# Optimization experiments

Measured on AMD Instinct MI355X. Metric: run time of the kernel, lower is better.

Reference implementation:

```python
import jax, jax.numpy as jnp
import numpy as np

NEG_SLOPE = 0.2


def _attn_layer(x, src, dst, W, a, n_nodes):
    # x: (N, Cin), W: (Cout, Cin) torch Linear convention, a: (2*Cout,)
    h = x @ W.T                                  # (N, Cout)
    H = h.shape[-1]
    # cat([x_i, x_j]) @ a  ==  h[dst] @ a[:H] + h[src] @ a[H:]
    s_i = h @ a[:H]                              # (N,)
    s_j = h @ a[H:]                              # (N,)
    score = s_i[dst] + s_j[src]                  # (E,)
    alpha = jax.nn.leaky_relu(score, NEG_SLOPE)
    # segment softmax over destination nodes
    amax = jax.ops.segment_max(alpha, dst, num_segments=n_nodes)
    amax = jnp.where(jnp.isfinite(amax), amax, 0.0)
    ex = jnp.exp(alpha - amax[dst])
    denom = jax.ops.segment_sum(ex, dst, num_segments=n_nodes)
    alpha = ex / denom[dst]                      # (E,)
    msg = h[src] * alpha[:, None]                # (E, Cout)
    sums = jax.ops.segment_sum(msg, dst, num_segments=n_nodes)
    cnt = jax.ops.segment_sum(jnp.ones_like(alpha), dst, num_segments=n_nodes)
    return sums / jnp.maximum(cnt, 1.0)[:, None]  # mean aggregation


def setup_inputs() -> dict:
    key = jax.random.key(0)
    ks = jax.random.split(key, 8)
    B, N, C, H, E = 16, 2048, 256, 256, 262144
    NT = B * N
    temporal_features = jax.random.normal(ks[0], (B, N, C), dtype=jnp.float32)
    edge_index = jax.random.randint(ks[1], (2, E), 0, NT, dtype=jnp.int64)
    sc = 1.0 / np.sqrt(C)
    W1 = jax.random.normal(ks[2], (H, C), dtype=jnp.float32) * sc
    a1 = jax.random.normal(ks[3], (2 * H,), dtype=jnp.float32) * sc
    W2 = jax.random.normal(ks[4], (H, H), dtype=jnp.float32) * sc
    a2 = jax.random.normal(ks[5], (2 * H,), dtype=jnp.float32) * sc
    W3 = jax.random.normal(ks[6], (H, H), dtype=jnp.float32) * sc
    a3 = jax.random.normal(ks[7], (2 * H,), dtype=jnp.float32) * sc
    return {"temporal_features": temporal_features, "edge_index": edge_index,
            "W1": W1, "a1": a1, "W2": W2, "a2": a2, "W3": W3, "a3": a3}


def reference(temporal_features, edge_index, W1, a1, W2, a2, W3, a3):
    B, N, C = temporal_features.shape
    n_nodes = B * N
    src, dst = edge_index[0], edge_index[1]  # x_j = x[src], x_i = x[dst]
    x = temporal_features.reshape(n_nodes, C)
    for W, a in ((W1, a1), (W2, a2), (W3, a3)):
        x = _attn_layer(x, src, dst, W, a, n_nodes)
        x = jax.nn.elu(x)
    return x.reshape(B, N, -1)
```

## Files before the change

### kernel.cpp

```cpp
#include <hip/hip_runtime.h>
#include <math.h>
#include <stdint.h>


typedef float f32x4 __attribute__((ext_vector_type(4)));
typedef _Float16 f16x8 __attribute__((ext_vector_type(8)));
typedef _Float16 f16x4 __attribute__((ext_vector_type(4)));

#define LDSPAD 40


__global__ __launch_bounds__(256) void convert_f16(const float* __restrict__ src,
                                                   _Float16* __restrict__ dstp)
{
    const int i = (blockIdx.x * 256 + threadIdx.x) * 8;
    float4 a = *(const float4*)&src[i];
    float4 b = *(const float4*)&src[i + 4];
    f16x8 o = {(_Float16)a.x, (_Float16)a.y, (_Float16)a.z, (_Float16)a.w,
               (_Float16)b.x, (_Float16)b.y, (_Float16)b.z, (_Float16)b.w};
    *(f16x8*)&dstp[i] = o;
}


__global__ __launch_bounds__(256) void gemm_f16(const _Float16* __restrict__ X,
                                                const _Float16* __restrict__ Wh,
                                                const float* __restrict__ avec,
                                                _Float16* __restrict__ Hout,
                                                float* __restrict__ si,
                                                float* __restrict__ sj)
{
    __shared__ __align__(16) unsigned char smem[64 * LDSPAD * 2 + 256 * LDSPAD * 2];
    _Float16* Xs = (_Float16*)smem;
    _Float16* Wl = (_Float16*)(smem + 64 * LDSPAD * 2);
    float*    Es = (float*)smem;

    const int tid  = threadIdx.x;
    const int lane = tid & 63;
    const int w    = tid >> 6;
    const int ln   = lane & 15;
    const int kq   = lane >> 4;
    const int m0   = blockIdx.x * 64;

    f32x4 acc[4][4] = {};

    const int sr = tid >> 2;
    const int sc = tid & 3;
    const _Float16* Xrow = X  + (size_t)(m0 + sr) * 256;
    const _Float16* Wrow = Wh + (size_t)tid * 256;

    for (int k0 = 0; k0 < 256; k0 += 32) {
        f16x8 xv = *(const f16x8*)&Xrow[k0 + sc * 8];
        *(f16x8*)&Xs[sr * LDSPAD + sc * 8] = xv;
        f16x8 w0 = *(const f16x8*)&Wrow[k0 + 0];
        f16x8 w1 = *(const f16x8*)&Wrow[k0 + 8];
        f16x8 w2 = *(const f16x8*)&Wrow[k0 + 16];
        f16x8 w3 = *(const f16x8*)&Wrow[k0 + 24];
        *(f16x8*)&Wl[tid * LDSPAD + 0]  = w0;
        *(f16x8*)&Wl[tid * LDSPAD + 8]  = w1;
        *(f16x8*)&Wl[tid * LDSPAD + 16] = w2;
        *(f16x8*)&Wl[tid * LDSPAD + 24] = w3;
        __syncthreads();

        f16x8 af[4], bf[4];
#pragma unroll
        for (int i = 0; i < 4; ++i)
            af[i] = *(const f16x8*)&Xs[(i * 16 + ln) * LDSPAD + kq * 8];
#pragma unroll
        for (int j = 0; j < 4; ++j)
            bf[j] = *(const f16x8*)&Wl[(w * 64 + j * 16 + ln) * LDSPAD + kq * 8];
#pragma unroll
        for (int i = 0; i < 4; ++i)
#pragma unroll
            for (int j = 0; j < 4; ++j)
                acc[i][j] = __builtin_amdgcn_mfma_f32_16x16x32_f16(af[i], bf[j], acc[i][j], 0, 0, 0);
        __syncthreads();
    }

    const int er = tid >> 4;
    const int ec = tid & 15;
    for (int i = 0; i < 4; ++i) {
#pragma unroll
        for (int j = 0; j < 4; ++j) {
            const int col = w * 64 + j * 16 + ln;
#pragma unroll
            for (int q = 0; q < 4; ++q)
                Es[(kq * 4 + q) * 260 + col] = acc[i][j][q];
        }
        __syncthreads();
        const int grow = m0 + i * 16 + er;
        float d0 = 0.f, d1 = 0.f;
#pragma unroll
        for (int c4 = 0; c4 < 4; ++c4) {
            const int col = ec * 4 + c4 * 64;
            f32x4 v  = *(const f32x4*)&Es[er * 260 + col];
            f16x4 hv = {(_Float16)v[0], (_Float16)v[1], (_Float16)v[2], (_Float16)v[3]};
            *(f16x4*)&Hout[(size_t)grow * 256 + col] = hv;
            f32x4 al = *(const f32x4*)&avec[col];
            f32x4 ah = *(const f32x4*)&avec[256 + col];
            d0 += v[0] * al[0] + v[1] * al[1] + v[2] * al[2] + v[3] * al[3];
            d1 += v[0] * ah[0] + v[1] * ah[1] + v[2] * ah[2] + v[3] * ah[3];
        }
#pragma unroll
        for (int d = 8; d; d >>= 1) {
            d0 += __shfl_xor(d0, d);
            d1 += __shfl_xor(d1, d);
        }
        if (ec == 0) { si[grow] = d0; sj[grow] = d1; }
        __syncthreads();
    }
}


__global__ void zero_int(int* p, int n)
{
    int i = blockIdx.x * blockDim.x + threadIdx.x;
    if (i < n) p[i] = 0;
}

__global__ void hist_kernel(const int* __restrict__ dst, int* __restrict__ cnt, int E)
{
    int e = blockIdx.x * blockDim.x + threadIdx.x;
    if (e < E) atomicAdd(&cnt[dst[e]], 1);
}

__global__ __launch_bounds__(1024) void scan_part(const int* __restrict__ cnt,
                                                  int* __restrict__ off,
                                                  int* __restrict__ bsum)
{
    __shared__ int buf[1024];
    const int tid = threadIdx.x;
    const int g = blockIdx.x * 1024 + tid;
    int v = cnt[g];
    buf[tid] = v;
    __syncthreads();
#pragma unroll
    for (int d = 1; d < 1024; d <<= 1) {
        int t = (tid >= d) ? buf[tid - d] : 0;
        __syncthreads();
        buf[tid] += t;
        __syncthreads();
    }
    off[g] = buf[tid] - v;
    if (tid == 1023) bsum[blockIdx.x] = buf[1023];
}

__global__ void scan_bsum(int* bsum, int nb)
{
    __shared__ int b[64];
    const int tid = threadIdx.x;
    b[tid] = (tid < nb) ? bsum[tid] : 0;
    __syncthreads();
    if (tid == 0) {
        int a = 0;
        for (int i = 0; i < nb; ++i) { int t = b[i]; b[i] = a; a += t; }
    }
    __syncthreads();
    if (tid < nb) bsum[tid] = b[tid];
}

__global__ __launch_bounds__(1024) void scan_add(const int* __restrict__ bsum,
                                                 int* __restrict__ off,
                                                 int* __restrict__ cursor,
                                                 int NT, int E)
{
    const int tid = threadIdx.x;
    const int g = blockIdx.x * 1024 + tid;
    int v = off[g] + bsum[blockIdx.x];
    off[g] = v;
    cursor[g] = v;
    if (g == 0) off[NT] = E;
}

__global__ void scatter_kernel(const int* __restrict__ src,
                               const int* __restrict__ dst,
                               int* __restrict__ cursor,
                               int* __restrict__ ssrc, int E)
{
    int e = blockIdx.x * blockDim.x + threadIdx.x;
    if (e < E) {
        int p = atomicAdd(&cursor[dst[e]], 1);
        ssrc[p] = src[e];
    }
}


__device__ __forceinline__ float bcast_f(float x, int l)
{
    return __uint_as_float(__builtin_amdgcn_readlane(__float_as_uint(x), l));
}

template <int F16OUT>
__global__ __launch_bounds__(256) void aggregate(const _Float16* __restrict__ Hh,
                                                 const float* __restrict__ si,
                                                 const float* __restrict__ sj,
                                                 const int* __restrict__ off,
                                                 const int* __restrict__ ssrc,
                                                 void* __restrict__ outv,
                                                 int n_nodes)
{
    const int v = (blockIdx.x * 256 + threadIdx.x) >> 6;
    const int lane = threadIdx.x & 63;
    if (v >= n_nodes) return;

    const int e0 = off[v], e1 = off[v + 1];
    const int deg = e1 - e0;
    f32x4 acc = {0.f, 0.f, 0.f, 0.f};

    if (deg > 0 && deg <= 64) {
        const float siv = si[v];
        const int idx = e0 + lane;
        const bool on = idx < e1;
        int s = 0;
        float scv = -1e30f;
        if (on) {
            s = ssrc[idx];
            float t = siv + sj[s];
            scv = (t >= 0.f) ? t : 0.2f * t;
        }
        float m = scv;
#pragma unroll
        for (int d = 32; d; d >>= 1) m = fmaxf(m, __shfl_xor(m, d));
        float wv = on ? __expf(scv - m) : 0.f;
        float den = wv;
#pragma unroll
        for (int d = 32; d; d >>= 1) den += __shfl_xor(den, d);

        const int c4 = lane * 4;
        for (int eo = 0; eo < deg; eo += 4) {
            const int l1 = (eo + 1 < 63) ? eo + 1 : 63;
            const int l2 = (eo + 2 < 63) ? eo + 2 : 63;
            const int l3 = (eo + 3 < 63) ? eo + 3 : 63;
            const int s0 = __builtin_amdgcn_readlane(s, eo);
            const int s1 = __builtin_amdgcn_readlane(s, l1);
            const int s2 = __builtin_amdgcn_readlane(s, l2);
            const int s3 = __builtin_amdgcn_readlane(s, l3);
            const float w0 = bcast_f(wv, eo);
            const float w1 = bcast_f(wv, l1);
            const float w2 = bcast_f(wv, l2);
            const float w3 = bcast_f(wv, l3);
            const f16x4 v0 = *(const f16x4*)&Hh[(size_t)s0 * 256 + c4];
            const f16x4 v1 = *(const f16x4*)&Hh[(size_t)s1 * 256 + c4];
            const f16x4 v2 = *(const f16x4*)&Hh[(size_t)s2 * 256 + c4];
            const f16x4 v3 = *(const f16x4*)&Hh[(size_t)s3 * 256 + c4];
#pragma unroll
            for (int q = 0; q < 4; ++q)
                acc[q] += w0 * (float)v0[q] + w1 * (float)v1[q]
                        + w2 * (float)v2[q] + w3 * (float)v3[q];
        }
        const float inv = 1.f / (den * (float)deg);
#pragma unroll
        for (int q = 0; q < 4; ++q) acc[q] *= inv;
    } else if (deg > 64) {
        const float siv = si[v];
        float m = -1e30f;
        for (int b = e0 + lane; b < e1; b += 64) {
            float t = siv + sj[ssrc[b]];
            t = (t >= 0.f) ? t : 0.2f * t;
            m = fmaxf(m, t);
        }
#pragma unroll
        for (int d = 32; d; d >>= 1) m = fmaxf(m, __shfl_xor(m, d));
        float den = 0.f;
        for (int b = e0 + lane; b < e1; b += 64) {
            float t = siv + sj[ssrc[b]];
            t = (t >= 0.f) ? t : 0.2f * t;
            den += __expf(t - m);
        }
#pragma unroll
        for (int d = 32; d; d >>= 1) den += __shfl_xor(den, d);
        for (int e = e0; e < e1; ++e) {
            const int s = ssrc[e];
            float t = siv + sj[s];
            t = (t >= 0.f) ? t : 0.2f * t;
            const float wgt = __expf(t - m);
            const f16x4 hv = *(const f16x4*)&Hh[(size_t)s * 256 + lane * 4];
#pragma unroll
            for (int q = 0; q < 4; ++q) acc[q] += wgt * (float)hv[q];
        }
        const float inv = 1.f / (den * (float)deg);
#pragma unroll
        for (int q = 0; q < 4; ++q) acc[q] *= inv;
    }

    float4 o;
    o.x = (acc[0] > 0.f) ? acc[0] : (__expf(acc[0]) - 1.f);
    o.y = (acc[1] > 0.f) ? acc[1] : (__expf(acc[1]) - 1.f);
    o.z = (acc[2] > 0.f) ? acc[2] : (__expf(acc[2]) - 1.f);
    o.w = (acc[3] > 0.f) ? acc[3] : (__expf(acc[3]) - 1.f);
    if (F16OUT) {
        f16x4 oh = {(_Float16)o.x, (_Float16)o.y, (_Float16)o.z, (_Float16)o.w};
        *(f16x4*)&((_Float16*)outv)[(size_t)v * 256 + lane * 4] = oh;
    } else {
        *(float4*)&((float*)outv)[(size_t)v * 256 + lane * 4] = o;
    }
}


extern "C" void kernel_launch(void* const* d_in, const int* in_sizes, int n_in,
                              void* d_out, int out_size, void* d_ws, size_t ws_size,
                              hipStream_t stream)
{
    const float* x0 = (const float*)d_in[0];
    const int*   ei = (const int*)d_in[1];
    const float* Ws[3] = {(const float*)d_in[2], (const float*)d_in[4], (const float*)d_in[6]};
    const float* as[3] = {(const float*)d_in[3], (const float*)d_in[5], (const float*)d_in[7]};
    float* out = (float*)d_out;

    const int NT = in_sizes[0] / 256;
    const int E  = in_sizes[1] / 2;
    const int* srcI = ei;
    const int* dstI = ei + E;

    _Float16* Hh = (_Float16*)d_ws;
    _Float16* Xh = Hh + (size_t)NT * 256;
    float* si    = (float*)(Xh + (size_t)NT * 256);
    float* sj    = si + NT;
    int* cnt     = (int*)(sj + NT);
    int* off     = cnt + NT;
    int* cursor  = off + NT + 1;
    int* ssrc    = cursor + NT;
    int* bsum    = ssrc + E;
    _Float16* Wh = (_Float16*)(((uintptr_t)(bsum + 64) + 255) & ~(uintptr_t)255);

    for (int l = 0; l < 3; ++l)
        convert_f16<<<32, 256, 0, stream>>>(Ws[l], Wh + (size_t)l * 65536);
    convert_f16<<<NT * 256 / 2048, 256, 0, stream>>>(x0, Xh);

    zero_int<<<(NT + 255) / 256, 256, 0, stream>>>(cnt, NT);
    hist_kernel<<<(E + 255) / 256, 256, 0, stream>>>(dstI, cnt, E);
    scan_part<<<NT / 1024, 1024, 0, stream>>>(cnt, off, bsum);
    scan_bsum<<<1, 64, 0, stream>>>(bsum, NT / 1024);
    scan_add<<<NT / 1024, 1024, 0, stream>>>(bsum, off, cursor, NT, E);
    scatter_kernel<<<(E + 255) / 256, 256, 0, stream>>>(srcI, dstI, cursor, ssrc, E);

    for (int l = 0; l < 3; ++l) {
        gemm_f16<<<NT / 64, 256, 0, stream>>>(Xh, Wh + (size_t)l * 65536, as[l], Hh, si, sj);
        if (l < 2)
            aggregate<1><<<NT / 4, 256, 0, stream>>>(Hh, si, sj, off, ssrc, (void*)Xh, NT);
        else
            aggregate<0><<<NT / 4, 256, 0, stream>>>(Hh, si, sj, off, ssrc, (void*)out, NT);
    }
}
```

Before: 266.5 us.

## Keep W fragments in registers and stream X directly from global in GEMM

The GEMM is restructured to use 512-thread blocks over 128 rows. Each wave preloads its 32-column slice of W for the full K into registers and streams X fragments straight from global memory with one-step prefetch. This removes the LDS staging and per-k-step barriers of the main loop. It costs higher register pressure (W fragments plus 16 accumulators) and uncoalesced strided global loads of X, and the epilogue is widened to 8-element f16 stores.

```diff
diff --git a/kernel.cpp b/kernel.cpp
--- a/kernel.cpp
+++ b/kernel.cpp
@@ -6,8 +6,6 @@
 typedef float f32x4 __attribute__((ext_vector_type(4)));
 typedef _Float16 f16x8 __attribute__((ext_vector_type(8)));
 typedef _Float16 f16x4 __attribute__((ext_vector_type(4)));
-
-#define LDSPAD 40
 
 
 __global__ __launch_bounds__(256) void convert_f16(const float* __restrict__ src,
@@ -22,86 +20,85 @@
 }
 
 
-__global__ __launch_bounds__(256) void gemm_f16(const _Float16* __restrict__ X,
-                                                const _Float16* __restrict__ Wh,
-                                                const float* __restrict__ avec,
-                                                _Float16* __restrict__ Hout,
-                                                float* __restrict__ si,
-                                                float* __restrict__ sj)
-{
-    __shared__ __align__(16) unsigned char smem[64 * LDSPAD * 2 + 256 * LDSPAD * 2];
-    _Float16* Xs = (_Float16*)smem;
-    _Float16* Wl = (_Float16*)(smem + 64 * LDSPAD * 2);
-    float*    Es = (float*)smem;
+__global__ __launch_bounds__(512, 2) void gemm_f16(const _Float16* __restrict__ X,
+                                                   const _Float16* __restrict__ Wh,
+                                                   const float* __restrict__ avec,
+                                                   _Float16* __restrict__ Hout,
+                                                   float* __restrict__ si,
+                                                   float* __restrict__ sj)
+{
+    __shared__ float Es[16][260];
 
     const int tid  = threadIdx.x;
     const int lane = tid & 63;
     const int w    = tid >> 6;
     const int ln   = lane & 15;
     const int kq   = lane >> 4;
-    const int m0   = blockIdx.x * 64;
-
-    f32x4 acc[4][4] = {};
-
-    const int sr = tid >> 2;
-    const int sc = tid & 3;
-    const _Float16* Xrow = X  + (size_t)(m0 + sr) * 256;
-    const _Float16* Wrow = Wh + (size_t)tid * 256;
-
-    for (int k0 = 0; k0 < 256; k0 += 32) {
-        f16x8 xv = *(const f16x8*)&Xrow[k0 + sc * 8];
-        *(f16x8*)&Xs[sr * LDSPAD + sc * 8] = xv;
-        f16x8 w0 = *(const f16x8*)&Wrow[k0 + 0];
-        f16x8 w1 = *(const f16x8*)&Wrow[k0 + 8];
-        f16x8 w2 = *(const f16x8*)&Wrow[k0 + 16];
-        f16x8 w3 = *(const f16x8*)&Wrow[k0 + 24];
-        *(f16x8*)&Wl[tid * LDSPAD + 0]  = w0;
-        *(f16x8*)&Wl[tid * LDSPAD + 8]  = w1;
-        *(f16x8*)&Wl[tid * LDSPAD + 16] = w2;
-        *(f16x8*)&Wl[tid * LDSPAD + 24] = w3;
-        __syncthreads();
-
-        f16x8 af[4], bf[4];
-#pragma unroll
-        for (int i = 0; i < 4; ++i)
-            af[i] = *(const f16x8*)&Xs[(i * 16 + ln) * LDSPAD + kq * 8];
-#pragma unroll
-        for (int j = 0; j < 4; ++j)
-            bf[j] = *(const f16x8*)&Wl[(w * 64 + j * 16 + ln) * LDSPAD + kq * 8];
-#pragma unroll
-        for (int i = 0; i < 4; ++i)
-#pragma unroll
-            for (int j = 0; j < 4; ++j)
-                acc[i][j] = __builtin_amdgcn_mfma_f32_16x16x32_f16(af[i], bf[j], acc[i][j], 0, 0, 0);
-        __syncthreads();
-    }
-
-    const int er = tid >> 4;
-    const int ec = tid & 15;
-    for (int i = 0; i < 4; ++i) {
-#pragma unroll
-        for (int j = 0; j < 4; ++j) {
-            const int col = w * 64 + j * 16 + ln;
+    const int m0   = blockIdx.x * 128;
+
+    f16x8 wf[2][8];
+#pragma unroll
+    for (int ks = 0; ks < 8; ++ks)
+#pragma unroll
+        for (int j = 0; j < 2; ++j)
+            wf[j][ks] = *(const f16x8*)&Wh[(size_t)(w * 32 + j * 16 + ln) * 256 + ks * 32 + kq * 8];
+
+    f32x4 acc[8][2] = {};
+    const _Float16* Xb = X + (size_t)m0 * 256 + kq * 8;
+
+    f16x8 xf[8];
+#pragma unroll
+    for (int i = 0; i < 8; ++i)
+        xf[i] = *(const f16x8*)&Xb[(size_t)(i * 16 + ln) * 256];
+
+#pragma unroll
+    for (int ks = 0; ks < 8; ++ks) {
+        f16x8 xn[8];
+        if (ks < 7) {
+#pragma unroll
+            for (int i = 0; i < 8; ++i)
+                xn[i] = *(const f16x8*)&Xb[(size_t)(i * 16 + ln) * 256 + (ks + 1) * 32];
+        }
+#pragma unroll
+        for (int i = 0; i < 8; ++i)
+#pragma unroll
+            for (int j = 0; j < 2; ++j)
+                acc[i][j] = __builtin_amdgcn_mfma_f32_16x16x32_f16(xf[i], wf[j][ks], acc[i][j], 0, 0, 0);
+        if (ks < 7) {
+#pragma unroll
+            for (int i = 0; i < 8; ++i) xf[i] = xn[i];
+        }
+    }
+
+    const int er = tid >> 5;
+    const int ec = tid & 31;
+    for (int i = 0; i < 8; ++i) {
+#pragma unroll
+        for (int j = 0; j < 2; ++j) {
+            const int col = w * 32 + j * 16 + ln;
 #pragma unroll
             for (int q = 0; q < 4; ++q)
-                Es[(kq * 4 + q) * 260 + col] = acc[i][j][q];
+                Es[kq * 4 + q][col] = acc[i][j][q];
         }
         __syncthreads();
         const int grow = m0 + i * 16 + er;
-        float d0 = 0.f, d1 = 0.f;
-#pragma unroll
-        for (int c4 = 0; c4 < 4; ++c4) {
-            const int col = ec * 4 + c4 * 64;
-            f32x4 v  = *(const f32x4*)&Es[er * 260 + col];
-            f16x4 hv = {(_Float16)v[0], (_Float16)v[1], (_Float16)v[2], (_Float16)v[3]};
-            *(f16x4*)&Hout[(size_t)grow * 256 + col] = hv;
-            f32x4 al = *(const f32x4*)&avec[col];
-            f32x4 ah = *(const f32x4*)&avec[256 + col];
-            d0 += v[0] * al[0] + v[1] * al[1] + v[2] * al[2] + v[3] * al[3];
-            d1 += v[0] * ah[0] + v[1] * ah[1] + v[2] * ah[2] + v[3] * ah[3];
-        }
-#pragma unroll
-        for (int d = 8; d; d >>= 1) {
+        const int c0 = ec * 8;
+        f32x4 v0 = *(const f32x4*)&Es[er][c0];
+        f32x4 v1 = *(const f32x4*)&Es[er][c0 + 4];
+        f16x8 ho = {(_Float16)v0[0], (_Float16)v0[1], (_Float16)v0[2], (_Float16)v0[3],
+                    (_Float16)v1[0], (_Float16)v1[1], (_Float16)v1[2], (_Float16)v1[3]};
+        *(f16x8*)&Hout[(size_t)grow * 256 + c0] = ho;
+
+        f32x4 al0 = *(const f32x4*)&avec[c0];
+        f32x4 al1 = *(const f32x4*)&avec[c0 + 4];
+        f32x4 ah0 = *(const f32x4*)&avec[256 + c0];
+        f32x4 ah1 = *(const f32x4*)&avec[256 + c0 + 4];
+        float d0 = v0[0]*al0[0] + v0[1]*al0[1] + v0[2]*al0[2] + v0[3]*al0[3]
+                 + v1[0]*al1[0] + v1[1]*al1[1] + v1[2]*al1[2] + v1[3]*al1[3];
+        float d1 = v0[0]*ah0[0] + v0[1]*ah0[1] + v0[2]*ah0[2] + v0[3]*ah0[3]
+                 + v1[0]*ah1[0] + v1[1]*ah1[1] + v1[2]*ah1[2] + v1[3]*ah1[3];
+#pragma unroll
+        for (int d = 16; d; d >>= 1) {
             d0 += __shfl_xor(d0, d);
             d1 += __shfl_xor(d1, d);
         }
@@ -334,7 +331,7 @@
     scatter_kernel<<<(E + 255) / 256, 256, 0, stream>>>(srcI, dstI, cursor, ssrc, E);
 
     for (int l = 0; l < 3; ++l) {
-        gemm_f16<<<NT / 64, 256, 0, stream>>>(Xh, Wh + (size_t)l * 65536, as[l], Hh, si, sj);
+        gemm_f16<<<NT / 128, 512, 0, stream>>>(Xh, Wh + (size_t)l * 65536, as[l], Hh, si, sj);
         if (l < 2)
             aggregate<1><<<NT / 4, 256, 0, stream>>>(Hh, si, sj, off, ssrc, (void*)Xh, NT);
         else
```

New measurement: 282.4 us. 1.06x slower.
